# Kernel tuning notes

Hardware: AMD Instinct MI355X
Metric: run time of the kernel (lower is better)

Reference implementation:

```python
import jax, jax.numpy as jnp
import numpy as np
from jax import lax

# Model dims (mamba_ssm defaults: d_state=16, d_conv=4, expand=2, dt_rank=ceil(d_model/16))
V = 16384       # vocab_size
D = 1024        # embedding_dim / d_model
C_CLS = 128     # num_CLS_classes
D_INNER = 2 * D # expand * d_model = 2048
N = 16          # d_state
K = 4           # d_conv
DT_RANK = (D + 15) // 16  # 64
B, L = 4, 512


def setup_inputs() -> dict:
    key = jax.random.key(0)
    ks = jax.random.split(key, 12)
    s = 0.02
    tokens = jax.random.randint(ks[0], (B, L), 0, V, dtype=jnp.int64)
    embedding = jax.random.normal(ks[1], (V, D), jnp.float32) * s
    in_proj_w = jax.random.normal(ks[2], (2 * D_INNER, D), jnp.float32) * s
    conv_w = jax.random.normal(ks[3], (D_INNER, 1, K), jnp.float32) * 0.1
    conv_b = jnp.zeros((D_INNER,), jnp.float32)
    x_proj_w = jax.random.normal(ks[4], (DT_RANK + 2 * N, D_INNER), jnp.float32) * s
    dt_proj_w = jax.random.normal(ks[5], (D_INNER, DT_RANK), jnp.float32) * s
    dt_proj_b = jax.random.uniform(ks[6], (D_INNER,), jnp.float32, -4.0, -2.0)  # softplus -> small dt
    A_log = jnp.log(jnp.broadcast_to(jnp.arange(1, N + 1, dtype=jnp.float32), (D_INNER, N)))
    D_param = jnp.ones((D_INNER,), jnp.float32)
    out_proj_w = jax.random.normal(ks[7], (D, D_INNER), jnp.float32) * s
    recon_w = jax.random.normal(ks[8], (V, D), jnp.float32) * s
    cls_w = jax.random.normal(ks[9], (C_CLS, D), jnp.float32) * s
    return dict(tokens=tokens, embedding=embedding, in_proj_w=in_proj_w,
                conv_w=conv_w, conv_b=conv_b, x_proj_w=x_proj_w,
                dt_proj_w=dt_proj_w, dt_proj_b=dt_proj_b, A_log=A_log,
                D_param=D_param, out_proj_w=out_proj_w, recon_w=recon_w, cls_w=cls_w)


def _mamba(h, in_proj_w, conv_w, conv_b, x_proj_w, dt_proj_w, dt_proj_b, A_log, D_param, out_proj_w):
    # h: (B, L, D)
    xz = jnp.einsum('bld,ed->ble', h, in_proj_w)          # (B, L, 2*D_INNER)
    x, z = jnp.split(xz, 2, axis=-1)                      # each (B, L, D_INNER)
    # causal depthwise conv1d along L
    xt = jnp.swapaxes(x, 1, 2)                            # (B, D_INNER, L)
    xt = lax.conv_general_dilated(xt, conv_w, window_strides=(1,),
                                  padding=[(K - 1, 0)],
                                  feature_group_count=D_INNER,
                                  dimension_numbers=('NCH', 'OIH', 'NCH'))
    xt = xt + conv_b[None, :, None]
    x = jax.nn.silu(jnp.swapaxes(xt, 1, 2))               # (B, L, D_INNER)
    # input-dependent dt, B, C
    x_dbl = jnp.einsum('bld,ed->ble', x, x_proj_w)        # (B, L, DT_RANK+2N)
    dt, Bm, Cm = jnp.split(x_dbl, [DT_RANK, DT_RANK + N], axis=-1)
    delta = jax.nn.softplus(jnp.einsum('blr,dr->bld', dt, dt_proj_w) + dt_proj_b)  # (B,L,D_INNER)
    A = -jnp.exp(A_log)                                   # (D_INNER, N)
    dA = jnp.exp(delta[..., None] * A)                    # (B,L,D_INNER,N)
    dBx = delta[..., None] * Bm[:, :, None, :] * x[..., None]  # (B,L,D_INNER,N)
    # selective scan over time (sequential recurrence)
    dA_t = jnp.swapaxes(dA, 0, 1)                         # (L,B,D_INNER,N)
    dBx_t = jnp.swapaxes(dBx, 0, 1)
    C_t = jnp.swapaxes(Cm, 0, 1)                          # (L,B,N)
    def step(hc, inp):
        a, bx, c = inp
        hc = a * hc + bx                                  # (B,D_INNER,N)
        y = jnp.einsum('bdn,bn->bd', hc, c)
        return hc, y
    h0 = jnp.zeros((x.shape[0], D_INNER, N), x.dtype)
    _, ys = lax.scan(step, h0, (dA_t, dBx_t, C_t))
    y = jnp.swapaxes(ys, 0, 1) + x * D_param              # (B,L,D_INNER)
    y = y * jax.nn.silu(z)
    return jnp.einsum('ble,de->bld', y, out_proj_w)       # (B,L,D)


def reference(tokens, embedding, in_proj_w, conv_w, conv_b, x_proj_w,
              dt_proj_w, dt_proj_b, A_log, D_param, out_proj_w, recon_w, cls_w):
    h = embedding[tokens]                                 # (B,L,D)
    h = _mamba(h, in_proj_w, conv_w, conv_b, x_proj_w, dt_proj_w, dt_proj_b,
               A_log, D_param, out_proj_w)
    recon = jnp.einsum('bld,vd->blv', h, recon_w)         # (B,L,V)
    pooled = h.mean(axis=1)                               # mean CLS pooling assumption
    cls = jnp.einsum('bd,cd->bc', pooled, cls_w)          # (B,C_CLS)
    return (recon, cls)
```

## Files before the change

kernel.cpp:

```cpp
#include <hip/hip_runtime.h>
#include <hip/hip_bf16.h>
#include <stdint.h>

#define DIN    2048
#define MROWS  2048
#define LSEQ   512
#define NV     16384
#define DMODEL 1024
#define NC     8
#define CL     64

typedef __attribute__((ext_vector_type(8))) short bf16x8;
typedef __attribute__((ext_vector_type(4))) float f32x4;

__device__ __forceinline__ uint16_t f2bf(float f) {
  uint32_t u = __builtin_bit_cast(uint32_t, f);
  u += 0x7fffu + ((u >> 16) & 1u);
  return (uint16_t)(u >> 16);
}
__device__ __forceinline__ float bf2f(uint16_t u) {
  return __builtin_bit_cast(float, (uint32_t)u << 16);
}

__device__ __forceinline__ void gld_lds16(const uint16_t* g, uint16_t* l) {
  __builtin_amdgcn_global_load_lds(
      (const __attribute__((address_space(1))) void*)g,
      (__attribute__((address_space(3))) void*)l,
      16, 0, 0);
}

__global__ __launch_bounds__(512, 2) void gemm256_bf16_kernel(
    const uint16_t* __restrict__ A, const uint16_t* __restrict__ B,
    float* __restrict__ C, int M, int N, int K)
{
  __shared__ uint16_t lds[4 * 16384];
  const int tid = threadIdx.x;
  const int w   = tid >> 6;
  const int l   = tid & 63;

  const int nwg = gridDim.x;
  const int cpx = nwg >> 3;
  const int swz = (blockIdx.x & 7) * cpx + (blockIdx.x >> 3);
  const int nmy = M >> 8;
  const int bm  = (swz % nmy) << 8;
  const int bn  = (swz / nmy) << 8;

  const int fr = l & 15;
  const int fg = l >> 4;
  const int wr = w >> 2;
  const int wc = w & 3;

  const int srow = l >> 2;
  const int kof  = (((l & 3) ^ ((l >> 3) & 3)) << 3);
  const int ar0  = (w * 2 + 0) * 16 + srow;
  const int ar1  = (w * 2 + 1) * 16 + srow;
  const uint16_t* Ag0 = A + (size_t)(bm + ar0) * K + kof;
  const uint16_t* Ag1 = A + (size_t)(bm + ar1) * K + kof;
  const uint16_t* Bg0 = B + (size_t)(bn + ar0) * K + kof;
  const uint16_t* Bg1 = B + (size_t)(bn + ar1) * K + kof;
  const int lA0 = (w * 2 + 0) * 512;
  const int lA1 = (w * 2 + 1) * 512;
  const int lB0 = 8192 + (w * 2 + 0) * 512;
  const int lB1 = 8192 + (w * 2 + 1) * 512;

  const int axr  = ((fg ^ ((fr >> 1) & 3)) << 3);
  const int aoff = (wr * 128 + fr) * 32 + axr;
  const int boff = 8192 + (wc * 64 + fr) * 32 + axr;

  f32x4 acc[8][4] = {};
  const int NT = K >> 5;

  auto stage = [&](int t) {
    const int sb = (t & 3) << 14;
    const int k0 = t << 5;
    gld_lds16(Ag0 + k0, lds + sb + lA0);
    gld_lds16(Ag1 + k0, lds + sb + lA1);
    gld_lds16(Bg0 + k0, lds + sb + lB0);
    gld_lds16(Bg1 + k0, lds + sb + lB1);
  };
  auto compute_tile = [&](int sb) {
    bf16x8 af[8], bfr[4];
#pragma unroll
    for (int mi = 0; mi < 8; ++mi)
      af[mi] = *(const bf16x8*)(lds + sb + aoff + mi * 512);
#pragma unroll
    for (int ni = 0; ni < 4; ++ni)
      bfr[ni] = *(const bf16x8*)(lds + sb + boff + ni * 512);
    __builtin_amdgcn_s_setprio(1);
#pragma unroll
    for (int mi = 0; mi < 8; ++mi)
#pragma unroll
      for (int ni = 0; ni < 4; ++ni)
        acc[mi][ni] = __builtin_amdgcn_mfma_f32_16x16x32_bf16(af[mi], bfr[ni], acc[mi][ni], 0, 0, 0);
    __builtin_amdgcn_s_setprio(0);
  };

  stage(0); stage(1); stage(2);
  asm volatile("s_waitcnt vmcnt(8)" ::: "memory");
  __builtin_amdgcn_s_barrier();

  for (int t = 0; t < NT - 3; ++t) {
    stage(t + 3);
    compute_tile((t & 3) << 14);
    asm volatile("s_waitcnt vmcnt(8)" ::: "memory");
    __builtin_amdgcn_s_barrier();
  }
  compute_tile(((NT - 3) & 3) << 14);
  asm volatile("s_waitcnt vmcnt(4)" ::: "memory");
  __builtin_amdgcn_s_barrier();
  compute_tile(((NT - 2) & 3) << 14);
  asm volatile("s_waitcnt vmcnt(0)" ::: "memory");
  __builtin_amdgcn_s_barrier();
  compute_tile(((NT - 1) & 3) << 14);

#pragma unroll
  for (int mi = 0; mi < 8; ++mi) {
    const int r0 = bm + wr * 128 + mi * 16 + fg * 4;
#pragma unroll
    for (int ni = 0; ni < 4; ++ni) {
      const int c0 = bn + wc * 64 + ni * 16 + fr;
#pragma unroll
      for (int r = 0; r < 4; ++r)
        C[(size_t)(r0 + r) * N + c0] = acc[mi][ni][r];
    }
  }
}

__global__ __launch_bounds__(256) void gemm_bf16_kernel(
    const uint16_t* __restrict__ A, const uint16_t* __restrict__ B,
    float* __restrict__ Cf, uint16_t* __restrict__ Cbf,
    int M, int N, int K, int kchunk, const float* __restrict__ bias)
{
  __shared__ uint16_t As[128 * 32];
  __shared__ uint16_t Bs[128 * 32];
  const int tid  = threadIdx.x;
  const int wid  = tid >> 6;
  const int lane = tid & 63;
  const int bm = blockIdx.y * 128;
  const int bn = blockIdx.x * 128;
  const int k_beg = blockIdx.z * kchunk;
  float* Cout = Cf + (size_t)blockIdx.z * M * N;

  const int fr = lane & 15;
  const int fg = lane >> 4;
  const int wm = (wid >> 1) * 64;
  const int wn = (wid & 1) * 64;

  const int srow = wid * 32 + (lane >> 2);
  const int skof = (((lane & 3) ^ ((lane >> 2) & 3)) << 3);
  const uint16_t* Ag = A + (size_t)(bm + srow) * K + skof;
  const uint16_t* Bg = B + (size_t)(bn + srow) * K + skof;
  uint16_t* Al = As + wid * 1024;
  uint16_t* Bl = Bs + wid * 1024;

  const int cxr = ((fg ^ (fr & 3)) << 3);

  f32x4 acc[4][4] = {};

  for (int k0 = 0; k0 < kchunk; k0 += 32) {
    const int kk = k_beg + k0;
    gld_lds16(Ag + kk, Al);
    gld_lds16(Ag + (size_t)16 * K + kk, Al + 512);
    gld_lds16(Bg + kk, Bl);
    gld_lds16(Bg + (size_t)16 * K + kk, Bl + 512);
    asm volatile("s_waitcnt vmcnt(0)" ::: "memory");
    __syncthreads();
    bf16x8 af[4], bfr[4];
#pragma unroll
    for (int i = 0; i < 4; ++i)
      af[i] = *(const bf16x8*)(As + (wm + i * 16 + fr) * 32 + cxr);
#pragma unroll
    for (int j = 0; j < 4; ++j)
      bfr[j] = *(const bf16x8*)(Bs + (wn + j * 16 + fr) * 32 + cxr);
#pragma unroll
    for (int i = 0; i < 4; ++i)
#pragma unroll
      for (int j = 0; j < 4; ++j)
        acc[i][j] = __builtin_amdgcn_mfma_f32_16x16x32_bf16(af[i], bfr[j], acc[i][j], 0, 0, 0);
    __syncthreads();
  }

#pragma unroll
  for (int i = 0; i < 4; ++i) {
    const int r0 = bm + wm + i * 16 + fg * 4;
#pragma unroll
    for (int j = 0; j < 4; ++j) {
      const int c0 = bn + wn + j * 16 + fr;
      const float bv = bias ? bias[c0] : 0.f;
#pragma unroll
      for (int r = 0; r < 4; ++r) {
        float v = acc[i][j][r];
        if (bias) {
          const float u = v + bv;
          v = (u > 20.f) ? u : log1pf(__expf(u));
        }
        if (Cbf) Cbf[(size_t)(r0 + r) * N + c0] = f2bf(v);
        else     Cout[(size_t)(r0 + r) * N + c0] = v;
      }
    }
  }
}

__global__ __launch_bounds__(256) void mega_cvt_kernel(
    const int* __restrict__ tok, const float* __restrict__ emb,
    const float* __restrict__ wi, const float* __restrict__ wo,
    const float* __restrict__ wdt, const float* __restrict__ wx,
    uint16_t* __restrict__ hb, uint16_t* __restrict__ wib,
    uint16_t* __restrict__ wob, uint16_t* __restrict__ wdtb,
    uint16_t* __restrict__ wxb)
{
  const int bid = blockIdx.x;
  if (bid < 2048) {
    const int m = bid;
    const int t = tok[m];
    const float4 v = ((const float4*)(emb + (size_t)t * DMODEL))[threadIdx.x];
    ((ushort4*)(hb + (size_t)m * DMODEL))[threadIdx.x] =
        make_ushort4(f2bf(v.x), f2bf(v.y), f2bf(v.z), f2bf(v.w));
  } else if (bid < 6144) {
    const int i = (bid - 2048) * 256 + threadIdx.x;
    const float4 v = ((const float4*)wi)[i];
    ((ushort4*)wib)[i] = make_ushort4(f2bf(v.x), f2bf(v.y), f2bf(v.z), f2bf(v.w));
  } else if (bid < 8192) {
    const int i = (bid - 6144) * 256 + threadIdx.x;
    const float4 v = ((const float4*)wo)[i];
    ((ushort4*)wob)[i] = make_ushort4(f2bf(v.x), f2bf(v.y), f2bf(v.z), f2bf(v.w));
  } else if (bid < 8320) {
    const int i = (bid - 8192) * 256 + threadIdx.x;
    const float4 v = ((const float4*)wdt)[i];
    ((ushort4*)wdtb)[i] = make_ushort4(f2bf(v.x), f2bf(v.y), f2bf(v.z), f2bf(v.w));
  } else {
    const int i = (bid - 8320) * 256 + threadIdx.x;
    const int r = i >> 9, c = i & 511;
    ushort4 o = make_ushort4(0, 0, 0, 0);
    if (r < 96) {
      const float4 v = ((const float4*)wx)[(size_t)r * 512 + c];
      o = make_ushort4(f2bf(v.x), f2bf(v.y), f2bf(v.z), f2bf(v.w));
    }
    ((ushort4*)wxb)[i] = o;
  }
}

__global__ __launch_bounds__(256) void reduce8_dt_kernel(
    const float* __restrict__ in, float* __restrict__ xdbl, uint16_t* __restrict__ dtb) {
  const int i = blockIdx.x * 256 + threadIdx.x;
  float s = 0.f;
#pragma unroll
  for (int z = 0; z < 8; ++z) s += in[i + (size_t)z * 262144];
  xdbl[i] = s;
  const int c = i & 127;
  if (c < 64) dtb[(i >> 7) * 64 + c] = f2bf(s);
}

__global__ __launch_bounds__(256) void cvt_bf16_kernel(
    const float* __restrict__ in, uint16_t* __restrict__ out, int n4) {
  const int i = blockIdx.x * 256 + threadIdx.x;
  if (i >= n4) return;
  const float4 v = ((const float4*)in)[i];
  ((ushort4*)out)[i] = make_ushort4(f2bf(v.x), f2bf(v.y), f2bf(v.z), f2bf(v.w));
}

__global__ __launch_bounds__(256) void conv_silu_kernel(
    const uint16_t* __restrict__ xzb, const float* __restrict__ cw, const float* __restrict__ cb,
    uint16_t* __restrict__ xcb)
{
  const int idx = blockIdx.x * 256 + threadIdx.x;
  const int d4  = idx & 511;
  const int m   = idx >> 9;
  const int l   = m & (LSEQ - 1);
  const int d   = d4 << 2;
  const float4 cbv = *(const float4*)(cb + d);
  float a0 = cbv.x, a1 = cbv.y, a2 = cbv.z, a3 = cbv.w;
  const float4 w0 = *(const float4*)(cw + (d + 0) * 4);
  const float4 w1 = *(const float4*)(cw + (d + 1) * 4);
  const float4 w2 = *(const float4*)(cw + (d + 2) * 4);
  const float4 w3 = *(const float4*)(cw + (d + 3) * 4);
  const float wj0[4] = {w0.x, w0.y, w0.z, w0.w};
  const float wj1[4] = {w1.x, w1.y, w1.z, w1.w};
  const float wj2[4] = {w2.x, w2.y, w2.z, w2.w};
  const float wj3[4] = {w3.x, w3.y, w3.z, w3.w};
#pragma unroll
  for (int j = 0; j < 4; ++j) {
    const int lj = l - 3 + j;
    if (lj >= 0) {
      const ushort4 x = *(const ushort4*)(xzb + (size_t)(m - 3 + j) * 4096 + d);
      a0 += wj0[j] * bf2f(x.x);
      a1 += wj1[j] * bf2f(x.y);
      a2 += wj2[j] * bf2f(x.z);
      a3 += wj3[j] * bf2f(x.w);
    }
  }
  const float r0 = a0 / (1.f + __expf(-a0));
  const float r1 = a1 / (1.f + __expf(-a1));
  const float r2 = a2 / (1.f + __expf(-a2));
  const float r3 = a3 / (1.f + __expf(-a3));
  *(ushort4*)(xcb + (size_t)m * DIN + d) = make_ushort4(f2bf(r0), f2bf(r1), f2bf(r2), f2bf(r3));
}

__global__ __launch_bounds__(256) void scan_partial_kernel(
    const uint16_t* __restrict__ delta_bf, const uint16_t* __restrict__ xcb,
    const float* __restrict__ xdbl, const float* __restrict__ A_log,
    float* __restrict__ Pb, float* __restrict__ Qb)
{
  const int c = blockIdx.x;
  const int d = blockIdx.y * 256 + threadIdx.x;
  const int b = blockIdx.z;
  float Arow[16], P[16], Q[16];
#pragma unroll
  for (int n = 0; n < 16; ++n) {
    Arow[n] = -expf(A_log[d * 16 + n]);
    P[n] = 1.f; Q[n] = 0.f;
  }
  const int l0 = c * CL;
  for (int li = 0; li < CL; ++li) {
    const int m = b * LSEQ + l0 + li;
    const float de = bf2f(delta_bf[(size_t)m * DIN + d]);
    const float xv = bf2f(xcb[(size_t)m * DIN + d]);
    const float dx = de * xv;
    const float4 B0 = *(const float4*)(xdbl + (size_t)m * 128 + 64);
    const float4 B1 = *(const float4*)(xdbl + (size_t)m * 128 + 68);
    const float4 B2 = *(const float4*)(xdbl + (size_t)m * 128 + 72);
    const float4 B3 = *(const float4*)(xdbl + (size_t)m * 128 + 76);
    const float bv[16] = {B0.x, B0.y, B0.z, B0.w, B1.x, B1.y, B1.z, B1.w,
                          B2.x, B2.y, B2.z, B2.w, B3.x, B3.y, B3.z, B3.w};
#pragma unroll
    for (int n = 0; n < 16; ++n) {
      const float a = __expf(de * Arow[n]);
      P[n] *= a;
      Q[n] = a * Q[n] + dx * bv[n];
    }
  }
  const size_t base = ((size_t)(b * NC + c) * 16) * DIN + d;
#pragma unroll
  for (int n = 0; n < 16; ++n) {
    Pb[base + (size_t)n * DIN] = P[n];
    Qb[base + (size_t)n * DIN] = Q[n];
  }
}

__global__ __launch_bounds__(256) void scan_bounds_kernel(
    const float* __restrict__ Pb, const float* __restrict__ Qb, float* __restrict__ Hi)
{
  const int i = blockIdx.x * 256 + threadIdx.x;
  const int b = i >> 15;
  const int r = i & 32767;
  float h = 0.f;
#pragma unroll
  for (int c = 0; c < NC; ++c) {
    const size_t o = ((size_t)(b * NC + c) << 15) + r;
    Hi[o] = h;
    h = Pb[o] * h + Qb[o];
  }
}

__global__ __launch_bounds__(256) void scan_final_kernel(
    const uint16_t* __restrict__ delta_bf, const uint16_t* __restrict__ xcb,
    const float* __restrict__ xdbl, const uint16_t* __restrict__ xzb,
    const float* __restrict__ A_log, const float* __restrict__ Dp,
    const float* __restrict__ Hi, uint16_t* __restrict__ yb)
{
  const int c = blockIdx.x;
  const int d = blockIdx.y * 256 + threadIdx.x;
  const int b = blockIdx.z;
  float Arow[16], h[16];
  const size_t base = ((size_t)(b * NC + c) * 16) * DIN + d;
#pragma unroll
  for (int n = 0; n < 16; ++n) {
    Arow[n] = -expf(A_log[d * 16 + n]);
    h[n] = Hi[base + (size_t)n * DIN];
  }
  const float dpd = Dp[d];
  const int l0 = c * CL;
  for (int li = 0; li < CL; ++li) {
    const int m = b * LSEQ + l0 + li;
    const float de = bf2f(delta_bf[(size_t)m * DIN + d]);
    const float xv = bf2f(xcb[(size_t)m * DIN + d]);
    const float dx = de * xv;
    const float4 B0 = *(const float4*)(xdbl + (size_t)m * 128 + 64);
    const float4 B1 = *(const float4*)(xdbl + (size_t)m * 128 + 68);
    const float4 B2 = *(const float4*)(xdbl + (size_t)m * 128 + 72);
    const float4 B3 = *(const float4*)(xdbl + (size_t)m * 128 + 76);
    const float4 C0 = *(const float4*)(xdbl + (size_t)m * 128 + 80);
    const float4 C1 = *(const float4*)(xdbl + (size_t)m * 128 + 84);
    const float4 C2 = *(const float4*)(xdbl + (size_t)m * 128 + 88);
    const float4 C3 = *(const float4*)(xdbl + (size_t)m * 128 + 92);
    const float bv[16] = {B0.x, B0.y, B0.z, B0.w, B1.x, B1.y, B1.z, B1.w,
                          B2.x, B2.y, B2.z, B2.w, B3.x, B3.y, B3.z, B3.w};
    const float cv[16] = {C0.x, C0.y, C0.z, C0.w, C1.x, C1.y, C1.z, C1.w,
                          C2.x, C2.y, C2.z, C2.w, C3.x, C3.y, C3.z, C3.w};
    float yp = 0.f;
#pragma unroll
    for (int n = 0; n < 16; ++n) {
      const float a = __expf(de * Arow[n]);
      h[n] = a * h[n] + dx * bv[n];
      yp += h[n] * cv[n];
    }
    const float z = bf2f(xzb[(size_t)m * 4096 + 2048 + d]);
    const float sil = z / (1.f + __expf(-z));
    yb[(size_t)m * DIN + d] = f2bf((yp + xv * dpd) * sil);
  }
}

__global__ __launch_bounds__(256) void pool1_kernel(
    const uint16_t* __restrict__ h2b, float* __restrict__ part) {
  const int b = blockIdx.x >> 4, s = blockIdx.x & 15;
  const int c = threadIdx.x * 4;
  const uint16_t* base = h2b + ((size_t)(b * LSEQ + s * 32)) * DMODEL + c;
  float a0 = 0, a1 = 0, a2 = 0, a3 = 0;
  for (int l = 0; l < 32; ++l) {
    const ushort4 v = *(const ushort4*)(base + (size_t)l * DMODEL);
    a0 += bf2f(v.x); a1 += bf2f(v.y); a2 += bf2f(v.z); a3 += bf2f(v.w);
  }
  *(float4*)(part + (size_t)blockIdx.x * DMODEL + c) = make_float4(a0, a1, a2, a3);
}

__global__ __launch_bounds__(256) void pool2_cls_kernel(
    const float* __restrict__ part, const float* __restrict__ w, float* __restrict__ out) {
  __shared__ float pl[DMODEL];
  const int b = blockIdx.x, t = threadIdx.x;
  float4 s = make_float4(0, 0, 0, 0);
  for (int k = 0; k < 16; ++k) {
    const float4 v = *(const float4*)(part + ((size_t)(b * 16 + k)) * DMODEL + t * 4);
    s.x += v.x; s.y += v.y; s.z += v.z; s.w += v.w;
  }
  const float inv = 1.f / (float)LSEQ;
  pl[t * 4 + 0] = s.x * inv; pl[t * 4 + 1] = s.y * inv;
  pl[t * 4 + 2] = s.z * inv; pl[t * 4 + 3] = s.w * inv;
  __syncthreads();
  if (t < 128) {
    const float* wr = w + (size_t)t * DMODEL;
    float acc = 0.f;
    for (int k = 0; k < DMODEL; ++k) acc += pl[k] * wr[k];
    out[b * 128 + t] = acc;
  }
}

extern "C" void kernel_launch(void* const* d_in, const int* in_sizes, int n_in,
                              void* d_out, int out_size, void* d_ws, size_t ws_size,
                              hipStream_t stream) {
  const int*   tokens    = (const int*)d_in[0];
  const float* embedding = (const float*)d_in[1];
  const float* in_proj_w = (const float*)d_in[2];
  const float* conv_w    = (const float*)d_in[3];
  const float* conv_b    = (const float*)d_in[4];
  const float* x_proj_w  = (const float*)d_in[5];
  const float* dt_proj_w = (const float*)d_in[6];
  const float* dt_proj_b = (const float*)d_in[7];
  const float* A_log     = (const float*)d_in[8];
  const float* D_param   = (const float*)d_in[9];
  const float* out_prj_w = (const float*)d_in[10];
  const float* recon_w   = (const float*)d_in[11];
  const float* cls_w     = (const float*)d_in[12];

  char* ws = (char*)d_ws;
  const size_t MB = 1024 * 1024;
  uint16_t* h_bf   = (uint16_t*)(ws + 0);
  uint16_t* w_in   = (uint16_t*)(ws + 4 * MB);
  uint16_t* xz_bf  = (uint16_t*)(ws + 12 * MB);
  uint16_t* xc_b   = (uint16_t*)(ws + 28 * MB);
  uint16_t* wx_bf  = (uint16_t*)(ws + 36 * MB);
  uint16_t* dt_bf  = (uint16_t*)(ws + 36 * MB + 512 * 1024);
  uint16_t* wdt_bf = (uint16_t*)(ws + 36 * MB + 768 * 1024);
  float*    xdbl   = (float*)(ws + 37 * MB);
  uint16_t* delt_b = (uint16_t*)(ws + 38 * MB);
  float*    kscr   = (float*)(ws + 46 * MB);
  uint16_t* y_bf   = (uint16_t*)(ws + 54 * MB);
  uint16_t* h2_bf  = (uint16_t*)(ws + 62 * MB);
  uint16_t* wout_bf= (uint16_t*)(ws + 66 * MB);
  float*    part   = (float*)(ws + 70 * MB);
  uint16_t* wrec_bf= (uint16_t*)(ws + 71 * MB);
  float*    Pbuf   = (float*)(ws + 46 * MB);
  float*    Qbuf   = (float*)(ws + 50 * MB);
  float*    Hinit  = (float*)(ws + 0);

  const int RECON = MROWS * NV;

  mega_cvt_kernel<<<dim3(8576), dim3(256), 0, stream>>>(
      tokens, embedding, in_proj_w, out_prj_w, dt_proj_w, x_proj_w,
      h_bf, w_in, wout_bf, wdt_bf, wx_bf);
  gemm_bf16_kernel<<<dim3(32, 16, 1), dim3(256), 0, stream>>>(h_bf, w_in, nullptr, xz_bf, MROWS, 4096, 1024, 1024, nullptr);
  conv_silu_kernel<<<dim3(4096), dim3(256), 0, stream>>>(xz_bf, conv_w, conv_b, xc_b);
  gemm_bf16_kernel<<<dim3(1, 16, 8), dim3(256), 0, stream>>>(xc_b, wx_bf, kscr, nullptr, MROWS, 128, 2048, 256, nullptr);
  reduce8_dt_kernel<<<dim3(1024), dim3(256), 0, stream>>>(kscr, xdbl, dt_bf);
  gemm_bf16_kernel<<<dim3(16, 16, 1), dim3(256), 0, stream>>>(dt_bf, wdt_bf, nullptr, delt_b, MROWS, DIN, 64, 64, dt_proj_b);
  scan_partial_kernel<<<dim3(NC, 8, 4), dim3(256), 0, stream>>>(delt_b, xc_b, xdbl, A_log, Pbuf, Qbuf);
  scan_bounds_kernel<<<dim3(512), dim3(256), 0, stream>>>(Pbuf, Qbuf, Hinit);
  scan_final_kernel<<<dim3(NC, 8, 4), dim3(256), 0, stream>>>(delt_b, xc_b, xdbl, xz_bf, A_log, D_param, Hinit, y_bf);
  gemm_bf16_kernel<<<dim3(8, 16, 1), dim3(256), 0, stream>>>(y_bf, wout_bf, nullptr, h2_bf, MROWS, 1024, 2048, 2048, nullptr);
  cvt_bf16_kernel<<<dim3(16384), dim3(256), 0, stream>>>(recon_w, wrec_bf, NV * 1024 / 4);
  gemm256_bf16_kernel<<<dim3(512), dim3(512), 0, stream>>>(h2_bf, wrec_bf, (float*)d_out, MROWS, NV, 1024);
  pool1_kernel<<<dim3(64), dim3(256), 0, stream>>>(h2_bf, part);
  pool2_cls_kernel<<<dim3(4), dim3(256), 0, stream>>>(part, cls_w, (float*)d_out + RECON);
}
```

Before: 371.9 us.

## Fuse recon weight bf16 conversion into GEMM and split-K the out_proj GEMM

The recon GEMM now reads the fp32 recon weights directly. Each thread loads them into registers, converts them to bf16 and writes them to LDS, overlapped with the MFMA work, which removes the separate conversion kernel and its 32MB bf16 round trip. In exchange the GEMM reads twice as many bytes for B, does extra VALU work, and relies on register-staged loads with changed waitcnt handling. Separately, the out_proj GEMM is split along K into two slices to double its grid size, followed by a small kernel that sums the two fp32 partials and converts to bf16.

```diff
diff --git a/kernel.cpp b/kernel.cpp
--- a/kernel.cpp
+++ b/kernel.cpp
@@ -29,8 +29,8 @@
       16, 0, 0);
 }
 
-__global__ __launch_bounds__(512, 2) void gemm256_bf16_kernel(
-    const uint16_t* __restrict__ A, const uint16_t* __restrict__ B,
+__global__ __launch_bounds__(512, 2) void gemm256_cvtB_kernel(
+    const uint16_t* __restrict__ A, const float* __restrict__ Bf,
     float* __restrict__ C, int M, int N, int K)
 {
   __shared__ uint16_t lds[4 * 16384];
@@ -56,8 +56,8 @@
   const int ar1  = (w * 2 + 1) * 16 + srow;
   const uint16_t* Ag0 = A + (size_t)(bm + ar0) * K + kof;
   const uint16_t* Ag1 = A + (size_t)(bm + ar1) * K + kof;
-  const uint16_t* Bg0 = B + (size_t)(bn + ar0) * K + kof;
-  const uint16_t* Bg1 = B + (size_t)(bn + ar1) * K + kof;
+  const float*    Bg0 = Bf + (size_t)(bn + ar0) * K + kof;
+  const float*    Bg1 = Bf + (size_t)(bn + ar1) * K + kof;
   const int lA0 = (w * 2 + 0) * 512;
   const int lA1 = (w * 2 + 1) * 512;
   const int lB0 = 8192 + (w * 2 + 0) * 512;
@@ -70,14 +70,6 @@
   f32x4 acc[8][4] = {};
   const int NT = K >> 5;
 
-  auto stage = [&](int t) {
-    const int sb = (t & 3) << 14;
-    const int k0 = t << 5;
-    gld_lds16(Ag0 + k0, lds + sb + lA0);
-    gld_lds16(Ag1 + k0, lds + sb + lA1);
-    gld_lds16(Bg0 + k0, lds + sb + lB0);
-    gld_lds16(Bg1 + k0, lds + sb + lB1);
-  };
   auto compute_tile = [&](int sb) {
     bf16x8 af[8], bfr[4];
 #pragma unroll
@@ -94,20 +86,51 @@
         acc[mi][ni] = __builtin_amdgcn_mfma_f32_16x16x32_bf16(af[mi], bfr[ni], acc[mi][ni], 0, 0, 0);
     __builtin_amdgcn_s_setprio(0);
   };
-
-  stage(0); stage(1); stage(2);
-  asm volatile("s_waitcnt vmcnt(8)" ::: "memory");
+  auto cvt_store = [&](int sb, float4 a, float4 b, float4 c, float4 d) {
+    bf16x8 v0, v1;
+    v0[0] = (short)f2bf(a.x); v0[1] = (short)f2bf(a.y);
+    v0[2] = (short)f2bf(a.z); v0[3] = (short)f2bf(a.w);
+    v0[4] = (short)f2bf(b.x); v0[5] = (short)f2bf(b.y);
+    v0[6] = (short)f2bf(b.z); v0[7] = (short)f2bf(b.w);
+    v1[0] = (short)f2bf(c.x); v1[1] = (short)f2bf(c.y);
+    v1[2] = (short)f2bf(c.z); v1[3] = (short)f2bf(c.w);
+    v1[4] = (short)f2bf(d.x); v1[5] = (short)f2bf(d.y);
+    v1[6] = (short)f2bf(d.z); v1[7] = (short)f2bf(d.w);
+    *(bf16x8*)(lds + sb + lB0 + l * 8) = v0;
+    *(bf16x8*)(lds + sb + lB1 + l * 8) = v1;
+  };
+
+  for (int p = 0; p < 3; ++p) {
+    const int k0p = p << 5;
+    const int sbp = p << 14;
+    const float4 rb0 = *(const float4*)(Bg0 + k0p);
+    const float4 rb1 = *(const float4*)(Bg0 + k0p + 4);
+    const float4 rb2 = *(const float4*)(Bg1 + k0p);
+    const float4 rb3 = *(const float4*)(Bg1 + k0p + 4);
+    gld_lds16(Ag0 + k0p, lds + sbp + lA0);
+    gld_lds16(Ag1 + k0p, lds + sbp + lA1);
+    cvt_store(sbp, rb0, rb1, rb2, rb3);
+  }
+  asm volatile("s_waitcnt lgkmcnt(0)" ::: "memory");
   __builtin_amdgcn_s_barrier();
 
   for (int t = 0; t < NT - 3; ++t) {
-    stage(t + 3);
+    const int tp = t + 3;
+    const int k0p = tp << 5;
+    const int sbp = (tp & 3) << 14;
+    const float4 rb0 = *(const float4*)(Bg0 + k0p);
+    const float4 rb1 = *(const float4*)(Bg0 + k0p + 4);
+    const float4 rb2 = *(const float4*)(Bg1 + k0p);
+    const float4 rb3 = *(const float4*)(Bg1 + k0p + 4);
+    gld_lds16(Ag0 + k0p, lds + sbp + lA0);
+    gld_lds16(Ag1 + k0p, lds + sbp + lA1);
     compute_tile((t & 3) << 14);
-    asm volatile("s_waitcnt vmcnt(8)" ::: "memory");
+    cvt_store(sbp, rb0, rb1, rb2, rb3);
+    asm volatile("s_waitcnt lgkmcnt(0)" ::: "memory");
+    __builtin_amdgcn_sched_barrier(0);
     __builtin_amdgcn_s_barrier();
   }
   compute_tile(((NT - 3) & 3) << 14);
-  asm volatile("s_waitcnt vmcnt(4)" ::: "memory");
-  __builtin_amdgcn_s_barrier();
   compute_tile(((NT - 2) & 3) << 14);
   asm volatile("s_waitcnt vmcnt(0)" ::: "memory");
   __builtin_amdgcn_s_barrier();
@@ -251,12 +274,11 @@
   if (c < 64) dtb[(i >> 7) * 64 + c] = f2bf(s);
 }
 
-__global__ __launch_bounds__(256) void cvt_bf16_kernel(
-    const float* __restrict__ in, uint16_t* __restrict__ out, int n4) {
+__global__ __launch_bounds__(256) void reduce2_bf16_kernel(
+    const float* __restrict__ in, uint16_t* __restrict__ outb, int n) {
   const int i = blockIdx.x * 256 + threadIdx.x;
-  if (i >= n4) return;
-  const float4 v = ((const float4*)in)[i];
-  ((ushort4*)out)[i] = make_ushort4(f2bf(v.x), f2bf(v.y), f2bf(v.z), f2bf(v.w));
+  if (i >= n) return;
+  outb[i] = f2bf(in[i] + in[i + (size_t)n]);
 }
 
 __global__ __launch_bounds__(256) void conv_silu_kernel(
@@ -467,7 +489,7 @@
   uint16_t* h2_bf  = (uint16_t*)(ws + 62 * MB);
   uint16_t* wout_bf= (uint16_t*)(ws + 66 * MB);
   float*    part   = (float*)(ws + 70 * MB);
-  uint16_t* wrec_bf= (uint16_t*)(ws + 71 * MB);
+  float*    kscr2  = (float*)(ws + 71 * MB);
   float*    Pbuf   = (float*)(ws + 46 * MB);
   float*    Qbuf   = (float*)(ws + 50 * MB);
   float*    Hinit  = (float*)(ws + 0);
@@ -485,9 +507,9 @@
   scan_partial_kernel<<<dim3(NC, 8, 4), dim3(256), 0, stream>>>(delt_b, xc_b, xdbl, A_log, Pbuf, Qbuf);
   scan_bounds_kernel<<<dim3(512), dim3(256), 0, stream>>>(Pbuf, Qbuf, Hinit);
   scan_final_kernel<<<dim3(NC, 8, 4), dim3(256), 0, stream>>>(delt_b, xc_b, xdbl, xz_bf, A_log, D_param, Hinit, y_bf);
-  gemm_bf16_kernel<<<dim3(8, 16, 1), dim3(256), 0, stream>>>(y_bf, wout_bf, nullptr, h2_bf, MROWS, 1024, 2048, 2048, nullptr);
-  cvt_bf16_kernel<<<dim3(16384), dim3(256), 0, stream>>>(recon_w, wrec_bf, NV * 1024 / 4);
-  gemm256_bf16_kernel<<<dim3(512), dim3(512), 0, stream>>>(h2_bf, wrec_bf, (float*)d_out, MROWS, NV, 1024);
+  gemm_bf16_kernel<<<dim3(8, 16, 2), dim3(256), 0, stream>>>(y_bf, wout_bf, kscr2, nullptr, MROWS, 1024, 2048, 1024, nullptr);
+  reduce2_bf16_kernel<<<dim3(8192), dim3(256), 0, stream>>>(kscr2, h2_bf, MROWS * 1024);
+  gemm256_cvtB_kernel<<<dim3(512), dim3(512), 0, stream>>>(h2_bf, recon_w, (float*)d_out, MROWS, NV, 1024);
   pool1_kernel<<<dim3(64), dim3(256), 0, stream>>>(h2_bf, part);
   pool2_cls_kernel<<<dim3(4), dim3(256), 0, stream>>>(part, cls_w, (float*)d_out + RECON);
 }
```

Result: slower. 388.7 us (+4.5%).
